# Kernel tuning notes

Hardware: AMD Instinct MI355X
Metric: run time of the kernel (lower is better)

Reference implementation:

```python
import jax, jax.numpy as jnp
import numpy as np

B, S, H = 1, 2048, 2560
NH, NKV, HD, FF = 20, 5, 128, 6912
EPS = 1e-5
ROPE_THETA = 500000.0


def rms_norm(x, w):
    return x * jax.lax.rsqrt(jnp.mean(x * x, axis=-1, keepdims=True) + EPS) * w


def bitlinear(x, w):
    # per-token int8 activation fake-quant
    s = jnp.clip(jnp.max(jnp.abs(x), axis=-1, keepdims=True), 1e-5, None)
    xq = jnp.clip(jnp.round(x * (127.0 / s)), -128.0, 127.0) * (s / 127.0)
    # per-tensor ternary weight fake-quant
    ws = jnp.clip(jnp.mean(jnp.abs(w)), 1e-5, None)
    wq = jnp.clip(jnp.round(w / ws), -1.0, 1.0) * ws
    return xq @ wq.T


def rotate_half(x):
    x1, x2 = jnp.split(x, 2, axis=-1)
    return jnp.concatenate([-x2, x1], axis=-1)


def setup_inputs() -> dict:
    key = jax.random.key(0)
    ks = jax.random.split(key, 8)
    std = 0.02
    hidden_states = jax.random.normal(ks[0], (B, S, H), jnp.float32)
    # real RoPE tables (the torch harness fed rand; we use the model's rope)
    pos = jnp.arange(S, dtype=jnp.float32)
    inv_freq = 1.0 / (ROPE_THETA ** (jnp.arange(0, HD, 2, dtype=jnp.float32) / HD))
    freqs = pos[:, None] * inv_freq[None, :]
    emb = jnp.concatenate([freqs, freqs], axis=-1)  # [S, HD]
    cos = jnp.cos(emb)[None]
    sin = jnp.sin(emb)[None]
    return {
        "hidden_states": hidden_states,
        "cos": cos,
        "sin": sin,
        "w_in_ln": jnp.ones((H,), jnp.float32),
        "w_q": jax.random.normal(ks[1], (NH * HD, H), jnp.float32) * std,
        "w_k": jax.random.normal(ks[2], (NKV * HD, H), jnp.float32) * std,
        "w_v": jax.random.normal(ks[3], (NKV * HD, H), jnp.float32) * std,
        "w_o": jax.random.normal(ks[4], (H, NH * HD), jnp.float32) * std,
        "w_attn_sub": jnp.ones((H,), jnp.float32),
        "w_post_ln": jnp.ones((H,), jnp.float32),
        "w_gate": jax.random.normal(ks[5], (FF, H), jnp.float32) * std,
        "w_up": jax.random.normal(ks[6], (FF, H), jnp.float32) * std,
        "w_ffn_sub": jnp.ones((FF,), jnp.float32),
        "w_down": jax.random.normal(ks[7], (H, FF), jnp.float32) * std,
    }


def reference(hidden_states, cos, sin, w_in_ln, w_q, w_k, w_v, w_o,
              w_attn_sub, w_post_ln, w_gate, w_up, w_ffn_sub, w_down):
    # --- self-attention block ---
    residual = hidden_states
    x = rms_norm(hidden_states, w_in_ln)
    q = bitlinear(x, w_q).reshape(B, S, NH, HD).transpose(0, 2, 1, 3)   # [B,NH,S,HD]
    k = bitlinear(x, w_k).reshape(B, S, NKV, HD).transpose(0, 2, 1, 3)  # [B,NKV,S,HD]
    v = bitlinear(x, w_v).reshape(B, S, NKV, HD).transpose(0, 2, 1, 3)
    c = cos[:, None]  # [B,1,S,HD]
    s = sin[:, None]
    q = q * c + rotate_half(q) * s
    k = k * c + rotate_half(k) * s
    k = jnp.repeat(k, NH // NKV, axis=1)  # GQA expand -> [B,NH,S,HD]
    v = jnp.repeat(v, NH // NKV, axis=1)
    scores = jnp.einsum('bhqd,bhkd->bhqk', q, k) / np.sqrt(HD).astype(np.float32)
    causal = jnp.tril(jnp.ones((S, S), bool))
    scores = jnp.where(causal, scores, jnp.float32(-1e30))
    attn = jax.nn.softmax(scores, axis=-1)
    o = jnp.einsum('bhqk,bhkd->bhqd', attn, v).transpose(0, 2, 1, 3).reshape(B, S, H)
    o = bitlinear(rms_norm(o, w_attn_sub), w_o)  # sub-norm before o_proj
    h = residual + o
    # --- MLP block (relu^2 gated) ---
    residual = h
    x = rms_norm(h, w_post_ln)
    g = bitlinear(x, w_gate)
    u = bitlinear(x, w_up)
    m = jnp.square(jax.nn.relu(g)) * u
    m = bitlinear(rms_norm(m, w_ffn_sub), w_down)  # sub-norm before down_proj
    return residual + m
```

## Files before the change

kernel.cpp:

```cpp
#include <hip/hip_runtime.h>

#define S_ 2048
#define H_ 2560
#define NH_ 20
#define NKV_ 5
#define HD_ 128
#define FF_ 6912
#define EPS_ 1e-5f

typedef __bf16 bf16;
typedef _Float16 f16;
typedef __bf16 bf16x8 __attribute__((ext_vector_type(8)));
typedef _Float16 f16x8 __attribute__((ext_vector_type(8)));
typedef float f32x4 __attribute__((ext_vector_type(4)));

__device__ inline float waveSum(float v) {
#pragma unroll
    for (int off = 32; off > 0; off >>= 1) v += __shfl_down(v, off);
    return v;
}
__device__ inline float waveMax(float v) {
#pragma unroll
    for (int off = 32; off > 0; off >>= 1) v = fmaxf(v, __shfl_down(v, off));
    return v;
}

__global__ void k_absmean(const float* __restrict__ w, int n, float* __restrict__ out) {
    __shared__ float red[4];
    float p = 0.f;
    for (int i = blockIdx.x * blockDim.x + threadIdx.x; i < n; i += gridDim.x * blockDim.x)
        p += fabsf(w[i]);
    p = waveSum(p);
    if ((threadIdx.x & 63) == 0) red[threadIdx.x >> 6] = p;
    __syncthreads();
    if (threadIdx.x == 0) atomicAdd(out, red[0] + red[1] + red[2] + red[3]);
}

__global__ void k_quant_w(const float* __restrict__ w, int n,
                          const float* __restrict__ sum, float inv_n,
                          bf16* __restrict__ wq) {
    float ws = fmaxf(sum[0] * inv_n, 1e-5f);
    for (int i = blockIdx.x * blockDim.x + threadIdx.x; i < n; i += gridDim.x * blockDim.x) {
        float q = rintf(w[i] / ws);
        q = fminf(fmaxf(q, -1.f), 1.f);
        wq[i] = (bf16)q;
    }
}

__global__ void k_rms_quant(const float* __restrict__ x, const float* __restrict__ wln,
                            int n, bf16* __restrict__ xq, float* __restrict__ a_scale) {
    extern __shared__ float sx[];
    float* red = sx + n;
    int row = blockIdx.x, tid = threadIdx.x;
    const float* xr = x + (size_t)row * n;
    float p = 0.f;
    for (int i = tid; i < n; i += 256) { float v = xr[i]; sx[i] = v; p += v * v; }
    p = waveSum(p);
    if ((tid & 63) == 0) red[tid >> 6] = p;
    __syncthreads();
    float ssum = red[0] + red[1] + red[2] + red[3];
    float rms = rsqrtf(ssum * (1.0f / n) + EPS_);
    __syncthreads();
    float mx = 0.f;
    for (int i = tid; i < n; i += 256) {
        float xv = sx[i] * rms * wln[i];
        sx[i] = xv;
        mx = fmaxf(mx, fabsf(xv));
    }
    mx = waveMax(mx);
    if ((tid & 63) == 0) red[tid >> 6] = mx;
    __syncthreads();
    float s = fmaxf(fmaxf(fmaxf(red[0], red[1]), fmaxf(red[2], red[3])), 1e-5f);
    if (tid == 0) a_scale[row] = s * (1.0f / 127.0f);
    float qs = 127.0f / s;
    for (int i = tid; i < n; i += 256) {
        float q = rintf(sx[i] * qs);
        q = fminf(fmaxf(q, -128.f), 127.f);
        xq[(size_t)row * n + i] = (bf16)q;
    }
}

__global__ __launch_bounds__(256) void k_gemm_bt(
    const bf16* __restrict__ A, const bf16* __restrict__ Bw,
    int M, int N, int K,
    const float* __restrict__ a_scale, const float* __restrict__ ws_sum, float inv_n,
    const float* __restrict__ add, const float* __restrict__ gprev,
    float* __restrict__ outF) {
    __shared__ bf16 As[128 * 72];
    __shared__ bf16 Bs[128 * 72];
    int tid = threadIdx.x;
    int lane = tid & 63, w = tid >> 6;
    int quad = lane >> 4, l15 = lane & 15;
    int wm = w >> 1, wn = w & 1;
    int m0 = blockIdx.y * 128, n0 = blockIdx.x * 128;
    f32x4 acc[4][4] = {};
    int ar = tid >> 3, ac = (tid & 7) * 8;
    const bf16* Ag = A + (size_t)m0 * K;
    const bf16* Bg = Bw + (size_t)n0 * K;
    for (int kt = 0; kt < K; kt += 64) {
        __syncthreads();
#pragma unroll
        for (int ppp = 0; ppp < 4; ppp++) {
            int r = ar + ppp * 32;
            *(bf16x8*)&As[r * 72 + ac] = *(const bf16x8*)(Ag + (size_t)r * K + kt + ac);
            *(bf16x8*)&Bs[r * 72 + ac] = *(const bf16x8*)(Bg + (size_t)r * K + kt + ac);
        }
        __syncthreads();
#pragma unroll
        for (int kc = 0; kc < 2; kc++) {
            bf16x8 af[4], bfr[4];
#pragma unroll
            for (int i = 0; i < 4; i++)
                af[i] = *(const bf16x8*)&As[(wm * 64 + i * 16 + l15) * 72 + kc * 32 + quad * 8];
#pragma unroll
            for (int j = 0; j < 4; j++)
                bfr[j] = *(const bf16x8*)&Bs[(wn * 64 + j * 16 + l15) * 72 + kc * 32 + quad * 8];
#pragma unroll
            for (int i = 0; i < 4; i++)
#pragma unroll
                for (int j = 0; j < 4; j++)
                    acc[i][j] = __builtin_amdgcn_mfma_f32_16x16x32_bf16(af[i], bfr[j], acc[i][j], 0, 0, 0);
        }
    }
    float ws = fmaxf(ws_sum[0] * inv_n, 1e-5f);
#pragma unroll
    for (int i = 0; i < 4; i++) {
        int rowb = m0 + wm * 64 + i * 16 + quad * 4;
#pragma unroll
        for (int j = 0; j < 4; j++) {
            int col = n0 + wn * 64 + j * 16 + l15;
#pragma unroll
            for (int r = 0; r < 4; r++) {
                int row = rowb + r;
                float val = a_scale[row] * ws * acc[i][j][r];
                size_t off = (size_t)row * N + col;
                if (add) val += add[off];
                if (gprev) {
                    float gv = fmaxf(gprev[off], 0.f);
                    val = gv * gv * val;
                }
                outF[off] = val;
            }
        }
    }
}

__global__ void k_rope_split(const float* __restrict__ xin, f16* __restrict__ xh,
                             f16* __restrict__ xl, const float* __restrict__ cosp,
                             const float* __restrict__ sinp, int nh) {
    int idx = blockIdx.x * 256 + threadIdx.x;
    int d = idx & 63;
    int t = idx >> 6;
    int h = t % nh;
    int s = t / nh;
    size_t base = (size_t)s * (nh * HD_) + h * HD_;
    float x1 = xin[base + d], x2 = xin[base + d + 64];
    float c1 = cosp[s * HD_ + d], s1 = sinp[s * HD_ + d];
    float c2 = cosp[s * HD_ + d + 64], s2 = sinp[s * HD_ + d + 64];
    float y1 = x1 * c1 - x2 * s1;
    float y2 = x2 * c2 + x1 * s2;
    f16 h1 = (f16)y1, h2 = (f16)y2;
    xh[base + d] = h1;
    xl[base + d] = (f16)(y1 - (float)h1);
    xh[base + d + 64] = h2;
    xl[base + d + 64] = (f16)(y2 - (float)h2);
}

__global__ void k_split(const float* __restrict__ x, f16* __restrict__ xh,
                        f16* __restrict__ xl, int n) {
    int i = blockIdx.x * 256 + threadIdx.x;
    if (i < n) {
        float v = x[i];
        f16 h = (f16)v;
        xh[i] = h;
        xl[i] = (f16)(v - (float)h);
    }
}

__global__ __launch_bounds__(256) void k_attn(
    const f16* __restrict__ qhp, const f16* __restrict__ qlp,
    const f16* __restrict__ khp, const f16* __restrict__ klp,
    const f16* __restrict__ vhp, const f16* __restrict__ vlp,
    float* __restrict__ o) {
    __shared__ f16 Kth[32][136], Ktl[32][136];
    __shared__ f16 Vth[128][40], Vtl[128][40];
    __shared__ f16 Pth[4][16][40], Ptl[4][16][40];
    int tid = threadIdx.x;
    int w = tid >> 6, lane = tid & 63, quad = lane >> 4, l15 = lane & 15;
    int head = blockIdx.y;
    int q0 = blockIdx.x * 64;
    int kvh = head >> 2;

    f16x8 qfh[4], qfl[4];
    {
        int qrow = q0 + w * 16 + l15;
        const f16* qp = qhp + (size_t)qrow * (NH_ * HD_) + head * HD_ + quad * 8;
        const f16* qp2 = qlp + (size_t)qrow * (NH_ * HD_) + head * HD_ + quad * 8;
#pragma unroll
        for (int kc = 0; kc < 4; kc++) {
            qfh[kc] = *(const f16x8*)(qp + kc * 32);
            qfl[kc] = *(const f16x8*)(qp2 + kc * 32);
        }
    }
    f32x4 oacc[8] = {};
    float m_i[4], l_i[4];
#pragma unroll
    for (int r = 0; r < 4; r++) { m_i[r] = -3.0e38f; l_i[r] = 0.f; }
    int sr = tid >> 3, scb = (tid & 7) * 16;
    int nkt = (q0 + 64) >> 5;
    for (int kt = 0; kt < nkt; kt++) {
        int key0 = kt * 32;
        __syncthreads();
        {
            size_t koff = (size_t)(key0 + sr) * (NKV_ * HD_) + kvh * HD_ + scb;
            *(f16x8*)&Kth[sr][scb] = *(const f16x8*)(khp + koff);
            *(f16x8*)&Kth[sr][scb + 8] = *(const f16x8*)(khp + koff + 8);
            *(f16x8*)&Ktl[sr][scb] = *(const f16x8*)(klp + koff);
            *(f16x8*)&Ktl[sr][scb + 8] = *(const f16x8*)(klp + koff + 8);
            f16x8 v0 = *(const f16x8*)(vhp + koff), v1 = *(const f16x8*)(vhp + koff + 8);
            f16x8 w0 = *(const f16x8*)(vlp + koff), w1 = *(const f16x8*)(vlp + koff + 8);
#pragma unroll
            for (int j = 0; j < 8; j++) {
                Vth[scb + j][sr] = v0[j];
                Vth[scb + 8 + j][sr] = v1[j];
                Vtl[scb + j][sr] = w0[j];
                Vtl[scb + 8 + j][sr] = w1[j];
            }
        }
        __syncthreads();
        f32x4 sc[2] = {};
#pragma unroll
        for (int kn = 0; kn < 2; kn++)
#pragma unroll
            for (int kc = 0; kc < 4; kc++) {
                f16x8 kfh = *(const f16x8*)&Kth[kn * 16 + l15][kc * 32 + quad * 8];
                f16x8 kfl = *(const f16x8*)&Ktl[kn * 16 + l15][kc * 32 + quad * 8];
                sc[kn] = __builtin_amdgcn_mfma_f32_16x16x32_f16(qfh[kc], kfh, sc[kn], 0, 0, 0);
                sc[kn] = __builtin_amdgcn_mfma_f32_16x16x32_f16(qfh[kc], kfl, sc[kn], 0, 0, 0);
                sc[kn] = __builtin_amdgcn_mfma_f32_16x16x32_f16(qfl[kc], kfh, sc[kn], 0, 0, 0);
            }
        const float scale = 0.08838834764831845f;
#pragma unroll
        for (int r = 0; r < 4; r++) {
            int qr = q0 + w * 16 + quad * 4 + r;
            float s0 = sc[0][r] * scale, s1 = sc[1][r] * scale;
            if (key0 + l15 > qr) s0 = -1e30f;
            if (key0 + 16 + l15 > qr) s1 = -1e30f;
            float mx = fmaxf(s0, s1);
#pragma unroll
            for (int off = 8; off > 0; off >>= 1) mx = fmaxf(mx, __shfl_xor(mx, off));
            float mnew = fmaxf(m_i[r], mx);
            float alpha = expf(m_i[r] - mnew);
            m_i[r] = mnew;
            l_i[r] *= alpha;
#pragma unroll
            for (int dn = 0; dn < 8; dn++) oacc[dn][r] *= alpha;
            float p0 = expf(s0 - mnew), p1 = expf(s1 - mnew);
            l_i[r] += p0 + p1;
            f16 ph0 = (f16)p0, ph1 = (f16)p1;
            Pth[w][quad * 4 + r][l15] = ph0;
            Pth[w][quad * 4 + r][16 + l15] = ph1;
            Ptl[w][quad * 4 + r][l15] = (f16)(p0 - (float)ph0);
            Ptl[w][quad * 4 + r][16 + l15] = (f16)(p1 - (float)ph1);
        }
        __syncthreads();
        f16x8 pfh = *(const f16x8*)&Pth[w][l15][quad * 8];
        f16x8 pfl = *(const f16x8*)&Ptl[w][l15][quad * 8];
#pragma unroll
        for (int dn = 0; dn < 8; dn++) {
            f16x8 vfh = *(const f16x8*)&Vth[dn * 16 + l15][quad * 8];
            f16x8 vfl = *(const f16x8*)&Vtl[dn * 16 + l15][quad * 8];
            oacc[dn] = __builtin_amdgcn_mfma_f32_16x16x32_f16(pfh, vfh, oacc[dn], 0, 0, 0);
            oacc[dn] = __builtin_amdgcn_mfma_f32_16x16x32_f16(pfh, vfl, oacc[dn], 0, 0, 0);
            oacc[dn] = __builtin_amdgcn_mfma_f32_16x16x32_f16(pfl, vfh, oacc[dn], 0, 0, 0);
        }
    }
    float linv[4];
#pragma unroll
    for (int r = 0; r < 4; r++) {
        float lt = l_i[r];
#pragma unroll
        for (int off = 8; off > 0; off >>= 1) lt += __shfl_xor(lt, off);
        linv[r] = 1.0f / lt;
    }
#pragma unroll
    for (int dn = 0; dn < 8; dn++)
#pragma unroll
        for (int r = 0; r < 4; r++) {
            int row = q0 + w * 16 + quad * 4 + r;
            o[(size_t)row * (NH_ * HD_) + head * HD_ + dn * 16 + l15] = oacc[dn][r] * linv[r];
        }
}

extern "C" void kernel_launch(void* const* d_in, const int* in_sizes, int n_in,
                              void* d_out, int out_size, void* d_ws, size_t ws_size,
                              hipStream_t stream) {
    const float* hidden   = (const float*)d_in[0];
    const float* cosp     = (const float*)d_in[1];
    const float* sinp     = (const float*)d_in[2];
    const float* w_in_ln  = (const float*)d_in[3];
    const float* w_q      = (const float*)d_in[4];
    const float* w_k      = (const float*)d_in[5];
    const float* w_v      = (const float*)d_in[6];
    const float* w_o      = (const float*)d_in[7];
    const float* w_attn   = (const float*)d_in[8];
    const float* w_post   = (const float*)d_in[9];
    const float* w_gate   = (const float*)d_in[10];
    const float* w_up     = (const float*)d_in[11];
    const float* w_ffn    = (const float*)d_in[12];
    const float* w_down   = (const float*)d_in[13];
    float* out = (float*)d_out;

    const size_t SH = (size_t)S_ * H_;
    const size_t SKV = (size_t)S_ * NKV_ * HD_;

    char* p = (char*)d_ws;
    auto alloc = [&](size_t b) { char* r = p; p += (b + 255) & ~(size_t)255; return r; };
    float* sums   = (float*)alloc(64 * 4);
    float* ascale = (float*)alloc(S_ * 4);
    bf16* wqb     = (bf16*)alloc((size_t)FF_ * H_ * 2);
    bf16* xq      = (bf16*)alloc(SH * 2);
    bf16* xqf     = (bf16*)alloc((size_t)S_ * FF_ * 2);
    float* hbuf   = (float*)alloc(SH * 4);
    char* reg     = alloc(62914560);
    float* q   = (float*)reg;
    float* kf  = (float*)(reg + 20971520);
    float* vf  = (float*)(reg + 26214400);
    f16* qhb   = (f16*)(reg + 31457280);
    f16* qlb   = (f16*)(reg + 41943040);
    f16* khb   = (f16*)(reg + 52428800);
    f16* klb   = (f16*)(reg + 55050240);
    f16* vhb   = (f16*)(reg + 57671680);
    f16* vlb   = (f16*)(reg + 60293120);
    float* ob  = (float*)reg;
    float* mbuf = (float*)reg;

    hipMemsetAsync(sums, 0, 64 * 4, stream);
    const int nQ = NH_ * HD_ * H_, nKV = NKV_ * HD_ * H_, nG = FF_ * H_;
    k_absmean<<<512, 256, 0, stream>>>(w_q, nQ, sums + 0);
    k_absmean<<<512, 256, 0, stream>>>(w_k, nKV, sums + 1);
    k_absmean<<<512, 256, 0, stream>>>(w_v, nKV, sums + 2);
    k_absmean<<<512, 256, 0, stream>>>(w_o, nQ, sums + 3);
    k_absmean<<<512, 256, 0, stream>>>(w_gate, nG, sums + 4);
    k_absmean<<<512, 256, 0, stream>>>(w_up, nG, sums + 5);
    k_absmean<<<512, 256, 0, stream>>>(w_down, nG, sums + 6);

    k_rms_quant<<<S_, 256, (H_ + 64) * 4, stream>>>(hidden, w_in_ln, H_, xq, ascale);

    k_quant_w<<<2048, 256, 0, stream>>>(w_q, nQ, sums + 0, 1.0f / nQ, wqb);
    k_gemm_bt<<<dim3(NH_ * HD_ / 128, S_ / 128), 256, 0, stream>>>(
        xq, wqb, S_, NH_ * HD_, H_, ascale, sums + 0, 1.0f / nQ, nullptr, nullptr, q);
    k_quant_w<<<2048, 256, 0, stream>>>(w_k, nKV, sums + 1, 1.0f / nKV, wqb);
    k_gemm_bt<<<dim3(NKV_ * HD_ / 128, S_ / 128), 256, 0, stream>>>(
        xq, wqb, S_, NKV_ * HD_, H_, ascale, sums + 1, 1.0f / nKV, nullptr, nullptr, kf);
    k_quant_w<<<2048, 256, 0, stream>>>(w_v, nKV, sums + 2, 1.0f / nKV, wqb);
    k_gemm_bt<<<dim3(NKV_ * HD_ / 128, S_ / 128), 256, 0, stream>>>(
        xq, wqb, S_, NKV_ * HD_, H_, ascale, sums + 2, 1.0f / nKV, nullptr, nullptr, vf);

    k_rope_split<<<S_ * NH_ * 64 / 256, 256, 0, stream>>>(q, qhb, qlb, cosp, sinp, NH_);
    k_rope_split<<<S_ * NKV_ * 64 / 256, 256, 0, stream>>>(kf, khb, klb, cosp, sinp, NKV_);
    k_split<<<(int)(SKV / 256), 256, 0, stream>>>(vf, vhb, vlb, (int)SKV);

    k_attn<<<dim3(S_ / 64, NH_), 256, 0, stream>>>(qhb, qlb, khb, klb, vhb, vlb, ob);

    k_rms_quant<<<S_, 256, (H_ + 64) * 4, stream>>>(ob, w_attn, H_, xq, ascale);
    k_quant_w<<<2048, 256, 0, stream>>>(w_o, nQ, sums + 3, 1.0f / nQ, wqb);
    k_gemm_bt<<<dim3(H_ / 128, S_ / 128), 256, 0, stream>>>(
        xq, wqb, S_, H_, NH_ * HD_, ascale, sums + 3, 1.0f / nQ, hidden, nullptr, hbuf);

    k_rms_quant<<<S_, 256, (H_ + 64) * 4, stream>>>(hbuf, w_post, H_, xq, ascale);
    k_quant_w<<<4096, 256, 0, stream>>>(w_gate, nG, sums + 4, 1.0f / nG, wqb);
    k_gemm_bt<<<dim3(FF_ / 128, S_ / 128), 256, 0, stream>>>(
        xq, wqb, S_, FF_, H_, ascale, sums + 4, 1.0f / nG, nullptr, nullptr, mbuf);
    k_quant_w<<<4096, 256, 0, stream>>>(w_up, nG, sums + 5, 1.0f / nG, wqb);
    k_gemm_bt<<<dim3(FF_ / 128, S_ / 128), 256, 0, stream>>>(
        xq, wqb, S_, FF_, H_, ascale, sums + 5, 1.0f / nG, nullptr, mbuf, mbuf);

    k_rms_quant<<<S_, 256, (FF_ + 64) * 4, stream>>>(mbuf, w_ffn, FF_, xqf, ascale);

    k_quant_w<<<4096, 256, 0, stream>>>(w_down, nG, sums + 6, 1.0f / nG, wqb);
    k_gemm_bt<<<dim3(H_ / 128, S_ / 128), 256, 0, stream>>>(
        xqf, wqb, S_, H_, FF_, ascale, sums + 6, 1.0f / nG, hbuf, nullptr, out);
}
```

Before: 1.783 ms.

## Vectorize elementwise kernels, pre-transpose V, reverse attention tile order, drop barrier

Vectorizes the weight absmean, ternary weight quantization and RMS-norm/activation quantization kernels with float4/bf16x8 accesses, and resizes their grids to match. Replaces the V hi/lo split kernel with a tiled transpose kernel that writes V in a [dim][seq] layout. Attention can then load V tiles with contiguous vector stores instead of scattered per-element LDS writes. Attention also processes query tiles in reverse order so the longest causal tiles are scheduled first. A block-wide barrier before the per-wave P-tile reads is removed, on the assumption that each wave only reads its own P tile.

```diff
diff --git a/kernel.cpp b/kernel.cpp
--- a/kernel.cpp
+++ b/kernel.cpp
@@ -10,6 +10,7 @@
 
 typedef __bf16 bf16;
 typedef _Float16 f16;
+typedef __bf16 bf16x4 __attribute__((ext_vector_type(4)));
 typedef __bf16 bf16x8 __attribute__((ext_vector_type(8)));
 typedef _Float16 f16x8 __attribute__((ext_vector_type(8)));
 typedef float f32x4 __attribute__((ext_vector_type(4)));
@@ -28,8 +29,12 @@
 __global__ void k_absmean(const float* __restrict__ w, int n, float* __restrict__ out) {
     __shared__ float red[4];
     float p = 0.f;
-    for (int i = blockIdx.x * blockDim.x + threadIdx.x; i < n; i += gridDim.x * blockDim.x)
-        p += fabsf(w[i]);
+    int n4 = n >> 2;
+    const float4* w4 = (const float4*)w;
+    for (int i = blockIdx.x * blockDim.x + threadIdx.x; i < n4; i += gridDim.x * blockDim.x) {
+        float4 v = w4[i];
+        p += fabsf(v.x) + fabsf(v.y) + fabsf(v.z) + fabsf(v.w);
+    }
     p = waveSum(p);
     if ((threadIdx.x & 63) == 0) red[threadIdx.x >> 6] = p;
     __syncthreads();
@@ -40,32 +45,51 @@
                           const float* __restrict__ sum, float inv_n,
                           bf16* __restrict__ wq) {
     float ws = fmaxf(sum[0] * inv_n, 1e-5f);
-    for (int i = blockIdx.x * blockDim.x + threadIdx.x; i < n; i += gridDim.x * blockDim.x) {
-        float q = rintf(w[i] / ws);
-        q = fminf(fmaxf(q, -1.f), 1.f);
-        wq[i] = (bf16)q;
+    int n8 = n >> 3;
+    const float4* w4 = (const float4*)w;
+    bf16x8* wq8 = (bf16x8*)wq;
+    for (int i = blockIdx.x * 256 + threadIdx.x; i < n8; i += gridDim.x * 256) {
+        float4 a = w4[i * 2], b = w4[i * 2 + 1];
+        bf16x8 o;
+        o[0] = (bf16)fminf(fmaxf(rintf(a.x / ws), -1.f), 1.f);
+        o[1] = (bf16)fminf(fmaxf(rintf(a.y / ws), -1.f), 1.f);
+        o[2] = (bf16)fminf(fmaxf(rintf(a.z / ws), -1.f), 1.f);
+        o[3] = (bf16)fminf(fmaxf(rintf(a.w / ws), -1.f), 1.f);
+        o[4] = (bf16)fminf(fmaxf(rintf(b.x / ws), -1.f), 1.f);
+        o[5] = (bf16)fminf(fmaxf(rintf(b.y / ws), -1.f), 1.f);
+        o[6] = (bf16)fminf(fmaxf(rintf(b.z / ws), -1.f), 1.f);
+        o[7] = (bf16)fminf(fmaxf(rintf(b.w / ws), -1.f), 1.f);
+        wq8[i] = o;
     }
 }
 
 __global__ void k_rms_quant(const float* __restrict__ x, const float* __restrict__ wln,
                             int n, bf16* __restrict__ xq, float* __restrict__ a_scale) {
     extern __shared__ float sx[];
-    float* red = sx + n;
+    __shared__ float red[4];
     int row = blockIdx.x, tid = threadIdx.x;
-    const float* xr = x + (size_t)row * n;
+    int n4 = n >> 2;
+    const float4* xr = (const float4*)(x + (size_t)row * n);
+    const float4* wl4 = (const float4*)wln;
+    float4* sx4 = (float4*)sx;
     float p = 0.f;
-    for (int i = tid; i < n; i += 256) { float v = xr[i]; sx[i] = v; p += v * v; }
+    for (int i = tid; i < n4; i += 256) {
+        float4 v = xr[i];
+        sx4[i] = v;
+        p += v.x * v.x + v.y * v.y + v.z * v.z + v.w * v.w;
+    }
     p = waveSum(p);
     if ((tid & 63) == 0) red[tid >> 6] = p;
     __syncthreads();
-    float ssum = red[0] + red[1] + red[2] + red[3];
-    float rms = rsqrtf(ssum * (1.0f / n) + EPS_);
+    float rms = rsqrtf((red[0] + red[1] + red[2] + red[3]) * (1.0f / n) + EPS_);
     __syncthreads();
     float mx = 0.f;
-    for (int i = tid; i < n; i += 256) {
-        float xv = sx[i] * rms * wln[i];
-        sx[i] = xv;
-        mx = fmaxf(mx, fabsf(xv));
+    for (int i = tid; i < n4; i += 256) {
+        float4 xv = sx4[i];
+        float4 wv = wl4[i];
+        xv.x *= rms * wv.x; xv.y *= rms * wv.y; xv.z *= rms * wv.z; xv.w *= rms * wv.w;
+        sx4[i] = xv;
+        mx = fmaxf(mx, fmaxf(fmaxf(fabsf(xv.x), fabsf(xv.y)), fmaxf(fabsf(xv.z), fabsf(xv.w))));
     }
     mx = waveMax(mx);
     if ((tid & 63) == 0) red[tid >> 6] = mx;
@@ -73,10 +97,15 @@
     float s = fmaxf(fmaxf(fmaxf(red[0], red[1]), fmaxf(red[2], red[3])), 1e-5f);
     if (tid == 0) a_scale[row] = s * (1.0f / 127.0f);
     float qs = 127.0f / s;
-    for (int i = tid; i < n; i += 256) {
-        float q = rintf(sx[i] * qs);
-        q = fminf(fmaxf(q, -128.f), 127.f);
-        xq[(size_t)row * n + i] = (bf16)q;
+    bf16x4* xo = (bf16x4*)(xq + (size_t)row * n);
+    for (int i = tid; i < n4; i += 256) {
+        float4 xv = sx4[i];
+        bf16x4 o;
+        o[0] = (bf16)fminf(fmaxf(rintf(xv.x * qs), -128.f), 127.f);
+        o[1] = (bf16)fminf(fmaxf(rintf(xv.y * qs), -128.f), 127.f);
+        o[2] = (bf16)fminf(fmaxf(rintf(xv.z * qs), -128.f), 127.f);
+        o[3] = (bf16)fminf(fmaxf(rintf(xv.w * qs), -128.f), 127.f);
+        xo[i] = o;
     }
 }
 
@@ -166,21 +195,39 @@
     xl[base + d + 64] = (f16)(y2 - (float)h2);
 }
 
-__global__ void k_split(const float* __restrict__ x, f16* __restrict__ xh,
-                        f16* __restrict__ xl, int n) {
-    int i = blockIdx.x * 256 + threadIdx.x;
-    if (i < n) {
-        float v = x[i];
-        f16 h = (f16)v;
-        xh[i] = h;
-        xl[i] = (f16)(v - (float)h);
+__global__ __launch_bounds__(256) void k_vtrans(const float* __restrict__ vf,
+                                                f16* __restrict__ vth, f16* __restrict__ vtl) {
+    __shared__ float tile[64][65];
+    int c0 = blockIdx.x * 64;
+    int s0 = blockIdx.y * 64;
+    int t = threadIdx.x;
+    int sl = t >> 2, cq = (t & 3) * 16;
+#pragma unroll
+    for (int i = 0; i < 16; i += 4)
+        *(float4*)&tile[sl][cq + i] =
+            *(const float4*)(vf + (size_t)(s0 + sl) * (NKV_ * HD_) + c0 + cq + i);
+    __syncthreads();
+    int cl = t >> 2, sq = (t & 3) * 16;
+#pragma unroll
+    for (int i = 0; i < 16; i += 8) {
+        f16x8 hi, lo;
+#pragma unroll
+        for (int j = 0; j < 8; j++) {
+            float v = tile[sq + i + j][cl];
+            f16 h = (f16)v;
+            hi[j] = h;
+            lo[j] = (f16)(v - (float)h);
+        }
+        size_t off = (size_t)(c0 + cl) * S_ + s0 + sq + i;
+        *(f16x8*)(vth + off) = hi;
+        *(f16x8*)(vtl + off) = lo;
     }
 }
 
 __global__ __launch_bounds__(256) void k_attn(
     const f16* __restrict__ qhp, const f16* __restrict__ qlp,
     const f16* __restrict__ khp, const f16* __restrict__ klp,
-    const f16* __restrict__ vhp, const f16* __restrict__ vlp,
+    const f16* __restrict__ vtg_h, const f16* __restrict__ vtg_l,
     float* __restrict__ o) {
     __shared__ f16 Kth[32][136], Ktl[32][136];
     __shared__ f16 Vth[128][40], Vtl[128][40];
@@ -188,18 +235,19 @@
     int tid = threadIdx.x;
     int w = tid >> 6, lane = tid & 63, quad = lane >> 4, l15 = lane & 15;
     int head = blockIdx.y;
-    int q0 = blockIdx.x * 64;
+    int qt = gridDim.x - 1 - blockIdx.x;
+    int q0 = qt * 64;
     int kvh = head >> 2;
+    const int KVSTR = NKV_ * HD_;
 
     f16x8 qfh[4], qfl[4];
     {
         int qrow = q0 + w * 16 + l15;
-        const f16* qp = qhp + (size_t)qrow * (NH_ * HD_) + head * HD_ + quad * 8;
-        const f16* qp2 = qlp + (size_t)qrow * (NH_ * HD_) + head * HD_ + quad * 8;
+        size_t qoff = (size_t)qrow * (NH_ * HD_) + head * HD_ + quad * 8;
 #pragma unroll
         for (int kc = 0; kc < 4; kc++) {
-            qfh[kc] = *(const f16x8*)(qp + kc * 32);
-            qfl[kc] = *(const f16x8*)(qp2 + kc * 32);
+            qfh[kc] = *(const f16x8*)(qhp + qoff + kc * 32);
+            qfl[kc] = *(const f16x8*)(qlp + qoff + kc * 32);
         }
     }
     f32x4 oacc[8] = {};
@@ -207,25 +255,22 @@
 #pragma unroll
     for (int r = 0; r < 4; r++) { m_i[r] = -3.0e38f; l_i[r] = 0.f; }
     int sr = tid >> 3, scb = (tid & 7) * 16;
+    int vd = tid >> 1, vh16 = (tid & 1) * 16;
     int nkt = (q0 + 64) >> 5;
     for (int kt = 0; kt < nkt; kt++) {
         int key0 = kt * 32;
         __syncthreads();
         {
-            size_t koff = (size_t)(key0 + sr) * (NKV_ * HD_) + kvh * HD_ + scb;
+            size_t koff = (size_t)(key0 + sr) * KVSTR + kvh * HD_ + scb;
             *(f16x8*)&Kth[sr][scb] = *(const f16x8*)(khp + koff);
             *(f16x8*)&Kth[sr][scb + 8] = *(const f16x8*)(khp + koff + 8);
             *(f16x8*)&Ktl[sr][scb] = *(const f16x8*)(klp + koff);
             *(f16x8*)&Ktl[sr][scb + 8] = *(const f16x8*)(klp + koff + 8);
-            f16x8 v0 = *(const f16x8*)(vhp + koff), v1 = *(const f16x8*)(vhp + koff + 8);
-            f16x8 w0 = *(const f16x8*)(vlp + koff), w1 = *(const f16x8*)(vlp + koff + 8);
-#pragma unroll
-            for (int j = 0; j < 8; j++) {
-                Vth[scb + j][sr] = v0[j];
-                Vth[scb + 8 + j][sr] = v1[j];
-                Vtl[scb + j][sr] = w0[j];
-                Vtl[scb + 8 + j][sr] = w1[j];
-            }
+            size_t voff = (size_t)(kvh * HD_ + vd) * S_ + key0 + vh16;
+            *(f16x8*)&Vth[vd][vh16] = *(const f16x8*)(vtg_h + voff);
+            *(f16x8*)&Vth[vd][vh16 + 8] = *(const f16x8*)(vtg_h + voff + 8);
+            *(f16x8*)&Vtl[vd][vh16] = *(const f16x8*)(vtg_l + voff);
+            *(f16x8*)&Vtl[vd][vh16 + 8] = *(const f16x8*)(vtg_l + voff + 8);
         }
         __syncthreads();
         f32x4 sc[2] = {};
@@ -263,7 +308,6 @@
             Ptl[w][quad * 4 + r][l15] = (f16)(p0 - (float)ph0);
             Ptl[w][quad * 4 + r][16 + l15] = (f16)(p1 - (float)ph1);
         }
-        __syncthreads();
         f16x8 pfh = *(const f16x8*)&Pth[w][l15][quad * 8];
         f16x8 pfl = *(const f16x8*)&Ptl[w][l15][quad * 8];
 #pragma unroll
@@ -312,7 +356,6 @@
     float* out = (float*)d_out;
 
     const size_t SH = (size_t)S_ * H_;
-    const size_t SKV = (size_t)S_ * NKV_ * HD_;
 
     char* p = (char*)d_ws;
     auto alloc = [&](size_t b) { char* r = p; p += (b + 255) & ~(size_t)255; return r; };
@@ -330,8 +373,8 @@
     f16* qlb   = (f16*)(reg + 41943040);
     f16* khb   = (f16*)(reg + 52428800);
     f16* klb   = (f16*)(reg + 55050240);
-    f16* vhb   = (f16*)(reg + 57671680);
-    f16* vlb   = (f16*)(reg + 60293120);
+    f16* vthb  = (f16*)(reg + 57671680);
+    f16* vtlb  = (f16*)(reg + 60293120);
     float* ob  = (float*)reg;
     float* mbuf = (float*)reg;
 
@@ -347,38 +390,38 @@
 
     k_rms_quant<<<S_, 256, (H_ + 64) * 4, stream>>>(hidden, w_in_ln, H_, xq, ascale);
 
-    k_quant_w<<<2048, 256, 0, stream>>>(w_q, nQ, sums + 0, 1.0f / nQ, wqb);
+    k_quant_w<<<3200, 256, 0, stream>>>(w_q, nQ, sums + 0, 1.0f / nQ, wqb);
     k_gemm_bt<<<dim3(NH_ * HD_ / 128, S_ / 128), 256, 0, stream>>>(
         xq, wqb, S_, NH_ * HD_, H_, ascale, sums + 0, 1.0f / nQ, nullptr, nullptr, q);
-    k_quant_w<<<2048, 256, 0, stream>>>(w_k, nKV, sums + 1, 1.0f / nKV, wqb);
+    k_quant_w<<<800, 256, 0, stream>>>(w_k, nKV, sums + 1, 1.0f / nKV, wqb);
     k_gemm_bt<<<dim3(NKV_ * HD_ / 128, S_ / 128), 256, 0, stream>>>(
         xq, wqb, S_, NKV_ * HD_, H_, ascale, sums + 1, 1.0f / nKV, nullptr, nullptr, kf);
-    k_quant_w<<<2048, 256, 0, stream>>>(w_v, nKV, sums + 2, 1.0f / nKV, wqb);
+    k_quant_w<<<800, 256, 0, stream>>>(w_v, nKV, sums + 2, 1.0f / nKV, wqb);
     k_gemm_bt<<<dim3(NKV_ * HD_ / 128, S_ / 128), 256, 0, stream>>>(
         xq, wqb, S_, NKV_ * HD_, H_, ascale, sums + 2, 1.0f / nKV, nullptr, nullptr, vf);
 
     k_rope_split<<<S_ * NH_ * 64 / 256, 256, 0, stream>>>(q, qhb, qlb, cosp, sinp, NH_);
     k_rope_split<<<S_ * NKV_ * 64 / 256, 256, 0, stream>>>(kf, khb, klb, cosp, sinp, NKV_);
-    k_split<<<(int)(SKV / 256), 256, 0, stream>>>(vf, vhb, vlb, (int)SKV);
-
-    k_attn<<<dim3(S_ / 64, NH_), 256, 0, stream>>>(qhb, qlb, khb, klb, vhb, vlb, ob);
+    k_vtrans<<<dim3(NKV_ * HD_ / 64, S_ / 64), 256, 0, stream>>>(vf, vthb, vtlb);
+
+    k_attn<<<dim3(S_ / 64, NH_), 256, 0, stream>>>(qhb, qlb, khb, klb, vthb, vtlb, ob);
 
     k_rms_quant<<<S_, 256, (H_ + 64) * 4, stream>>>(ob, w_attn, H_, xq, ascale);
-    k_quant_w<<<2048, 256, 0, stream>>>(w_o, nQ, sums + 3, 1.0f / nQ, wqb);
+    k_quant_w<<<3200, 256, 0, stream>>>(w_o, nQ, sums + 3, 1.0f / nQ, wqb);
     k_gemm_bt<<<dim3(H_ / 128, S_ / 128), 256, 0, stream>>>(
         xq, wqb, S_, H_, NH_ * HD_, ascale, sums + 3, 1.0f / nQ, hidden, nullptr, hbuf);
 
     k_rms_quant<<<S_, 256, (H_ + 64) * 4, stream>>>(hbuf, w_post, H_, xq, ascale);
-    k_quant_w<<<4096, 256, 0, stream>>>(w_gate, nG, sums + 4, 1.0f / nG, wqb);
+    k_quant_w<<<8640, 256, 0, stream>>>(w_gate, nG, sums + 4, 1.0f / nG, wqb);
     k_gemm_bt<<<dim3(FF_ / 128, S_ / 128), 256, 0, stream>>>(
         xq, wqb, S_, FF_, H_, ascale, sums + 4, 1.0f / nG, nullptr, nullptr, mbuf);
-    k_quant_w<<<4096, 256, 0, stream>>>(w_up, nG, sums + 5, 1.0f / nG, wqb);
+    k_quant_w<<<8640, 256, 0, stream>>>(w_up, nG, sums + 5, 1.0f / nG, wqb);
     k_gemm_bt<<<dim3(FF_ / 128, S_ / 128), 256, 0, stream>>>(
         xq, wqb, S_, FF_, H_, ascale, sums + 5, 1.0f / nG, nullptr, mbuf, mbuf);
 
     k_rms_quant<<<S_, 256, (FF_ + 64) * 4, stream>>>(mbuf, w_ffn, FF_, xqf, ascale);
 
-    k_quant_w<<<4096, 256, 0, stream>>>(w_down, nG, sums + 6, 1.0f / nG, wqb);
+    k_quant_w<<<8640, 256, 0, stream>>>(w_down, nG, sums + 6, 1.0f / nG, wqb);
     k_gemm_bt<<<dim3(H_ / 128, S_ / 128), 256, 0, stream>>>(
         xqf, wqb, S_, H_, FF_, ascale, sums + 6, 1.0f / nG, hbuf, nullptr, out);
 }
```

Measured after the change: 1.429 ms. 1.25x faster.
